# Kernel optimization log

Measured on AMD Instinct MI355X. Metric: run time of the kernel, lower is better.

Reference implementation:

```python
import jax, jax.numpy as jnp
import numpy as np

B, N, F, T, KCHEB, O = 8, 1024, 64, 12, 3, 64

def setup_inputs() -> dict:
    key = jax.random.key(0)
    k1, k2, k3, k4 = jax.random.split(key, 4)
    graph_signal = jax.random.normal(k1, (B, N, F, T), dtype=jnp.float32)
    spatial_attention = jax.random.uniform(k2, (B, N, N), dtype=jnp.float32)
    # Chebyshev polynomials of scaled Laplacian, scaled to keep magnitudes sane
    cheb = jax.random.normal(k3, (KCHEB, N, N), dtype=jnp.float32) / np.float32(np.sqrt(N))
    # theta: (K, F, num_of_filters), glorot-ish scale
    theta = jax.random.normal(k4, (KCHEB, F, O), dtype=jnp.float32) / np.float32(np.sqrt(F))
    return {"graph_signal": graph_signal, "spatial_attention": spatial_attention,
            "cheb": cheb, "theta": theta}

def reference(graph_signal, spatial_attention, cheb, theta):
    # Original loops over t and k computing:
    #   rhs[b,n,f] = sum_m (T_k[m,n] * att[b,m,n]) * x[b,m,f,t]   (transposed batch_dot)
    #   out[b,n,o,t] += rhs @ theta[k]
    # Vectorized over k, t in one pass.
    Ak = cheb[:, None, :, :] * spatial_attention[None]          # (K,B,N,N) = T_k * attention
    rhs = jnp.einsum('kbmn,bmft->kbnft', Ak, graph_signal)      # T_k_with_at^T @ x for all t
    out = jnp.einsum('kbnft,kfo->bnot', rhs, theta)             # sum over k and f
    return jax.nn.relu(out)                                     # (B, N, O, T)
```

## Files before the change

kernel.cpp:

```cpp
#include <hip/hip_runtime.h>
#include <stdint.h>

#define NB 8
#define NN 1024
#define NF 64
#define NT 12
#define NK 3
#define NO 64
#define NQ 768
#define KKC 3072

typedef __attribute__((ext_vector_type(8))) short bf16x8;
typedef __attribute__((ext_vector_type(4))) float f32x4;

typedef const unsigned int __attribute__((address_space(1)))* gas1_t;
typedef unsigned int __attribute__((address_space(3)))* las3_t;

__device__ __forceinline__ void gload_lds16(const void* g, void* l) {
  __builtin_amdgcn_global_load_lds((gas1_t)g, (las3_t)l, 16, 0, 0);
}

__device__ __forceinline__ unsigned short f2bf(float f) {
  union { float f; unsigned int u; } v; v.f = f;
  unsigned int u = v.u;
  unsigned int r = (u + 0x7FFFu + ((u >> 16) & 1u)) >> 16;
  return (unsigned short)r;
}

__global__ void k0_thetaT(const float* __restrict__ theta, unsigned short* __restrict__ thT) {
  int i = blockIdx.x * 256 + threadIdx.x;
  if (i >= NK * NO * NF) return;
  int f = i & 63, o = (i >> 6) & 63, k = i >> 12;
  thT[i] = f2bf(theta[(k * NF + f) * NO + o]);
}

__global__ __launch_bounds__(256) void k1_A2(const float* __restrict__ cheb,
                                             const float* __restrict__ att,
                                             unsigned short* __restrict__ A2) {
  __shared__ float att_s[64][65];
  __shared__ float cheb_s[64][65];
  const int n0 = blockIdx.x * 64;
  const int m0 = blockIdx.y * 64;
  const int b  = blockIdx.z;
  const int tid = threadIdx.x;
  const int r4 = tid >> 4;
  const int c  = tid & 15;

#pragma unroll
  for (int p = 0; p < 4; ++p) {
    int r = r4 + p * 16;
    const float4 v = *(const float4*)(att + ((size_t)(b * NN + m0 + r)) * NN + n0 + c * 4);
    att_s[r][c * 4 + 0] = v.x; att_s[r][c * 4 + 1] = v.y;
    att_s[r][c * 4 + 2] = v.z; att_s[r][c * 4 + 3] = v.w;
  }
  for (int k = 0; k < NK; ++k) {
#pragma unroll
    for (int p = 0; p < 4; ++p) {
      int r = r4 + p * 16;
      const float4 v = *(const float4*)(cheb + ((size_t)(k * NN + m0 + r)) * NN + n0 + c * 4);
      cheb_s[r][c * 4 + 0] = v.x; cheb_s[r][c * 4 + 1] = v.y;
      cheb_s[r][c * 4 + 2] = v.z; cheb_s[r][c * 4 + 3] = v.w;
    }
    __syncthreads();
#pragma unroll
    for (int p = 0; p < 8; ++p) {
      int e  = p * 256 + tid;
      int jn = e >> 5;
      int q  = e & 31;
      float f0 = att_s[2 * q][jn]     * cheb_s[2 * q][jn];
      float f1 = att_s[2 * q + 1][jn] * cheb_s[2 * q + 1][jn];
      unsigned int pk = (unsigned int)f2bf(f0) | ((unsigned int)f2bf(f1) << 16);
      size_t el = ((size_t)(b * NN + n0 + jn)) * KKC + k * NN + m0 + 2 * q;
      *(unsigned int*)(A2 + el) = pk;
    }
    __syncthreads();
  }
}

__global__ __launch_bounds__(256) void k2_xT(const float* __restrict__ x,
                                             unsigned short* __restrict__ xT) {
  __shared__ unsigned int lds[12][16][32];
  const int m0 = blockIdx.x * 16;
  const int b  = blockIdx.y;
  const int tid = threadIdx.x;
  const float* xb = x + ((size_t)(b * NN + m0)) * (NF * NT);

#pragma unroll
  for (int u0 = 0; u0 < 2; ++u0) {
    const int u  = u0 * 256 + tid;
    const int ml = u >> 5;
    const int fp = u & 31;
    const float* src = xb + ((size_t)ml * NF + fp * 2) * NT;
    float v[24];
#pragma unroll
    for (int i = 0; i < 6; ++i)
      *(float4*)(v + i * 4) = *(const float4*)(src + i * 4);
#pragma unroll
    for (int t = 0; t < 12; ++t) {
      unsigned int pk = (unsigned int)f2bf(v[t]) | ((unsigned int)f2bf(v[t + 12]) << 16);
      lds[t][ml][fp] = pk;
    }
  }
  __syncthreads();

#pragma unroll
  for (int it = 0; it < 12; ++it) {
    const int g = it * 256 + tid;
    const int t = g >> 8;
    const int r = g & 255;
    const int m = r >> 4;
    const int f4 = r & 15;
    uint2 u = *(const uint2*)&lds[t][m][2 * f4];
    size_t el = (((size_t)(b * NT + t) * NN) + m0 + m) * NF + f4 * 4;
    *(uint2*)(void*)(xT + el) = u;
  }
}

__global__ __launch_bounds__(256) void k3_Y(const unsigned short* __restrict__ xT,
                                            const unsigned short* __restrict__ thT,
                                            unsigned short* __restrict__ Y) {
  __shared__ unsigned short Xs[256 * 64];
  const int mc = blockIdx.x;
  const int t  = blockIdx.y;
  const int b  = blockIdx.z;
  const int tid = threadIdx.x;
  const int w = tid >> 6, l = tid & 63;
  const int lrow = l & 15, lk = l >> 4;

  const unsigned short* xbase = xT + ((size_t)(b * NT + t)) * NN * NF + (size_t)(mc * 256) * NF;

#pragma unroll
  for (int it = 0; it < 8; ++it) {
    const int idx = it * 256 + tid;
    const int r   = idx >> 3;
    const int c16 = (idx & 7) ^ (r & 7);
    gload_lds16(xbase + (size_t)r * NF + c16 * 8, Xs + (size_t)idx * 8);
  }
  __syncthreads();

  bf16x8 af[2][4];
#pragma unroll
  for (int ks = 0; ks < 2; ++ks)
#pragma unroll
    for (int mi = 0; mi < 4; ++mi) {
      const int row = w * 64 + mi * 16 + lrow;
      const int sw = (row * 128 + ks * 64 + lk * 16) ^ ((row & 7) << 4);
      af[ks][mi] = *(const bf16x8*)((const char*)Xs + sw);
    }

  for (int k = 0; k < NK; ++k) {
    const unsigned short* tb = thT + (size_t)k * NO * NF;
    f32x4 acc[4][4] = {};
#pragma unroll
    for (int ks = 0; ks < 2; ++ks) {
      bf16x8 bb[4];
#pragma unroll
      for (int oj = 0; oj < 4; ++oj)
        bb[oj] = *(const bf16x8*)(tb + (size_t)(oj * 16 + lrow) * NF + ks * 32 + lk * 8);
#pragma unroll
      for (int mi = 0; mi < 4; ++mi)
#pragma unroll
        for (int oj = 0; oj < 4; ++oj)
          acc[mi][oj] = __builtin_amdgcn_mfma_f32_16x16x32_bf16(af[ks][mi], bb[oj], acc[mi][oj], 0, 0, 0);
    }
#pragma unroll
    for (int mi = 0; mi < 4; ++mi) {
#pragma unroll
      for (int oj = 0; oj < 4; ++oj) {
        const int o  = oj * 16 + lrow;
        const int mg = mc * 256 + w * 64 + mi * 16 + lk * 4;
        uint2 u;
        u.x = (unsigned int)f2bf(acc[mi][oj][0]) | ((unsigned int)f2bf(acc[mi][oj][1]) << 16);
        u.y = (unsigned int)f2bf(acc[mi][oj][2]) | ((unsigned int)f2bf(acc[mi][oj][3]) << 16);
        size_t el = ((size_t)(b * NQ + o * NT + t)) * KKC + k * NN + mg;
        *(uint2*)(void*)(Y + el) = u;
      }
    }
  }
}

__global__ __launch_bounds__(256) void k4_main(const unsigned short* __restrict__ A2,
                                               const unsigned short* __restrict__ Y,
                                               float* __restrict__ out) {
  __shared__ unsigned short Asl[2][64 * 64];
  __shared__ unsigned short Bsl[2][128 * 64];
  const int tid = threadIdx.x;
  const int w = tid >> 6, l = tid & 63;
  const int lrow = l & 15, lk = l >> 4;
  const int wm = w >> 1, wq = w & 1;

  const int lin = (blockIdx.x & 7) * 96 + (blockIdx.x >> 3);
  const int b   = lin / 96;
  const int rem = lin % 96;
  const int bn  = rem / 6;
  const int bq  = rem % 6;

  const unsigned short* Abase = A2 + ((size_t)(b * NN + bn * 64)) * KKC;
  const unsigned short* Bbase = Y  + ((size_t)(b * NQ + bq * 128)) * KKC;

  f32x4 acc[2][4] = {};

  auto STAGE = [&](unsigned short* Ad, unsigned short* Bd, int kt) {
    const int kb = kt * 64;
#pragma unroll
    for (int it = 0; it < 2; ++it) {
      const int idx = it * 256 + tid;
      const int r   = idx >> 3;
      const int c16 = (idx & 7) ^ (r & 7);
      gload_lds16(Abase + (size_t)r * KKC + kb + c16 * 8, Ad + (size_t)idx * 8);
    }
#pragma unroll
    for (int it = 0; it < 4; ++it) {
      const int idx = it * 256 + tid;
      const int r   = idx >> 3;
      const int c16 = (idx & 7) ^ (r & 7);
      gload_lds16(Bbase + (size_t)r * KKC + kb + c16 * 8, Bd + (size_t)idx * 8);
    }
  };

  auto COMPUTE = [&](const unsigned short* As, const unsigned short* Bs) {
#pragma unroll
    for (int kss = 0; kss < 2; ++kss) {
      bf16x8 af[2], bfr[4];
#pragma unroll
      for (int mi = 0; mi < 2; ++mi) {
        const int row = wm * 32 + mi * 16 + lrow;
        const int sw = (row * 128 + kss * 64 + lk * 16) ^ ((row & 7) << 4);
        af[mi] = *(const bf16x8*)((const char*)As + sw);
      }
#pragma unroll
      for (int nj = 0; nj < 4; ++nj) {
        const int row = wq * 64 + nj * 16 + lrow;
        const int sw = (row * 128 + kss * 64 + lk * 16) ^ ((row & 7) << 4);
        bfr[nj] = *(const bf16x8*)((const char*)Bs + sw);
      }
#pragma unroll
      for (int mi = 0; mi < 2; ++mi)
#pragma unroll
        for (int nj = 0; nj < 4; ++nj)
          acc[mi][nj] = __builtin_amdgcn_mfma_f32_16x16x32_bf16(af[mi], bfr[nj], acc[mi][nj], 0, 0, 0);
    }
  };

  STAGE(Asl[0], Bsl[0], 0);
  for (int kt = 0; kt < KKC / 64; ++kt) {
    const int p = kt & 1;
    if (kt + 1 < KKC / 64) {
      STAGE(Asl[p ^ 1], Bsl[p ^ 1], kt + 1);
      asm volatile("s_waitcnt vmcnt(6)" ::: "memory");
    } else {
      asm volatile("s_waitcnt vmcnt(0)" ::: "memory");
    }
    __builtin_amdgcn_s_barrier();
    COMPUTE(Asl[p], Bsl[p]);
    __builtin_amdgcn_s_barrier();
  }

  const int nb0 = bn * 64 + wm * 32;
  const int qb0 = bq * 128 + wq * 64;
#pragma unroll
  for (int mi = 0; mi < 2; ++mi) {
#pragma unroll
    for (int nj = 0; nj < 4; ++nj) {
      const int q = qb0 + nj * 16 + lrow;
#pragma unroll
      for (int j = 0; j < 4; ++j) {
        const int n = nb0 + mi * 16 + lk * 4 + j;
        float v = acc[mi][nj][j];
        out[((size_t)(b * NN + n)) * NQ + q] = v > 0.f ? v : 0.f;
      }
    }
  }
}

extern "C" void kernel_launch(void* const* d_in, const int* in_sizes, int n_in,
                              void* d_out, int out_size, void* d_ws, size_t ws_size,
                              hipStream_t stream) {
  const float* x     = (const float*)d_in[0];
  const float* att   = (const float*)d_in[1];
  const float* cheb  = (const float*)d_in[2];
  const float* theta = (const float*)d_in[3];
  float* out = (float*)d_out;

  char* ws = (char*)d_ws;
  unsigned short* A2  = (unsigned short*)(ws);
  unsigned short* xT  = (unsigned short*)(ws + 50331648);
  unsigned short* Y   = (unsigned short*)(ws + 62914560);
  unsigned short* thT = (unsigned short*)(ws + 100663296);

  k0_thetaT<<<48, 256, 0, stream>>>(theta, thT);
  k1_A2<<<dim3(16, 16, 8), 256, 0, stream>>>(cheb, att, A2);
  k2_xT<<<dim3(64, 8), 256, 0, stream>>>(x, xT);
  k3_Y<<<dim3(4, 12, 8), 256, 0, stream>>>(xT, thT, Y);
  k4_main<<<768, 256, 0, stream>>>(A2, Y, out);
}
```

Baseline: 104.7 us.

## Reuse cheb tiles across batch in A2 build and enlarge main GEMM tiles

The A2 preparation kernel now loads all three Chebyshev tiles once per block and loops over the batch inside the block, so cheb is read from global memory once instead of once per batch. The grid shrinks from 2048 to 256 blocks. The main GEMM moves from 64x128 tiles with 256 threads to 128x192 tiles with 512 threads, giving each wave a 64x48 subtile for more operand reuse per LDS load. The trade-off is fewer blocks (256, roughly one per CU), more LDS per block, and less parallelism in the A2 kernel.

```diff
diff --git a/kernel.cpp b/kernel.cpp
--- a/kernel.cpp
+++ b/kernel.cpp
@@ -38,42 +38,46 @@
                                              const float* __restrict__ att,
                                              unsigned short* __restrict__ A2) {
   __shared__ float att_s[64][65];
-  __shared__ float cheb_s[64][65];
+  __shared__ float cheb_s[3][64][65];
   const int n0 = blockIdx.x * 64;
   const int m0 = blockIdx.y * 64;
-  const int b  = blockIdx.z;
   const int tid = threadIdx.x;
   const int r4 = tid >> 4;
   const int c  = tid & 15;
 
 #pragma unroll
-  for (int p = 0; p < 4; ++p) {
-    int r = r4 + p * 16;
-    const float4 v = *(const float4*)(att + ((size_t)(b * NN + m0 + r)) * NN + n0 + c * 4);
-    att_s[r][c * 4 + 0] = v.x; att_s[r][c * 4 + 1] = v.y;
-    att_s[r][c * 4 + 2] = v.z; att_s[r][c * 4 + 3] = v.w;
-  }
-  for (int k = 0; k < NK; ++k) {
+  for (int k = 0; k < NK; ++k)
 #pragma unroll
     for (int p = 0; p < 4; ++p) {
       int r = r4 + p * 16;
       const float4 v = *(const float4*)(cheb + ((size_t)(k * NN + m0 + r)) * NN + n0 + c * 4);
-      cheb_s[r][c * 4 + 0] = v.x; cheb_s[r][c * 4 + 1] = v.y;
-      cheb_s[r][c * 4 + 2] = v.z; cheb_s[r][c * 4 + 3] = v.w;
-    }
+      cheb_s[k][r][c * 4 + 0] = v.x; cheb_s[k][r][c * 4 + 1] = v.y;
+      cheb_s[k][r][c * 4 + 2] = v.z; cheb_s[k][r][c * 4 + 3] = v.w;
+    }
+
+  for (int b = 0; b < NB; ++b) {
     __syncthreads();
 #pragma unroll
-    for (int p = 0; p < 8; ++p) {
-      int e  = p * 256 + tid;
-      int jn = e >> 5;
-      int q  = e & 31;
-      float f0 = att_s[2 * q][jn]     * cheb_s[2 * q][jn];
-      float f1 = att_s[2 * q + 1][jn] * cheb_s[2 * q + 1][jn];
-      unsigned int pk = (unsigned int)f2bf(f0) | ((unsigned int)f2bf(f1) << 16);
-      size_t el = ((size_t)(b * NN + n0 + jn)) * KKC + k * NN + m0 + 2 * q;
-      *(unsigned int*)(A2 + el) = pk;
+    for (int p = 0; p < 4; ++p) {
+      int r = r4 + p * 16;
+      const float4 v = *(const float4*)(att + ((size_t)(b * NN + m0 + r)) * NN + n0 + c * 4);
+      att_s[r][c * 4 + 0] = v.x; att_s[r][c * 4 + 1] = v.y;
+      att_s[r][c * 4 + 2] = v.z; att_s[r][c * 4 + 3] = v.w;
     }
     __syncthreads();
+    for (int k = 0; k < NK; ++k) {
+#pragma unroll
+      for (int p = 0; p < 8; ++p) {
+        int e  = p * 256 + tid;
+        int jn = e >> 5;
+        int q  = e & 31;
+        float f0 = att_s[2 * q][jn]     * cheb_s[k][2 * q][jn];
+        float f1 = att_s[2 * q + 1][jn] * cheb_s[k][2 * q + 1][jn];
+        unsigned int pk = (unsigned int)f2bf(f0) | ((unsigned int)f2bf(f1) << 16);
+        size_t el = ((size_t)(b * NN + n0 + jn)) * KKC + k * NN + m0 + 2 * q;
+        *(unsigned int*)(A2 + el) = pk;
+      }
+    }
   }
 }
 
@@ -179,89 +183,89 @@
   }
 }
 
-__global__ __launch_bounds__(256) void k4_main(const unsigned short* __restrict__ A2,
+__global__ __launch_bounds__(512) void k4_main(const unsigned short* __restrict__ A2,
                                                const unsigned short* __restrict__ Y,
                                                float* __restrict__ out) {
-  __shared__ unsigned short Asl[2][64 * 64];
-  __shared__ unsigned short Bsl[2][128 * 64];
+  __shared__ unsigned short Asl[2][128 * 64];
+  __shared__ unsigned short Bsl[2][192 * 64];
   const int tid = threadIdx.x;
   const int w = tid >> 6, l = tid & 63;
   const int lrow = l & 15, lk = l >> 4;
-  const int wm = w >> 1, wq = w & 1;
-
-  const int lin = (blockIdx.x & 7) * 96 + (blockIdx.x >> 3);
-  const int b   = lin / 96;
-  const int rem = lin % 96;
-  const int bn  = rem / 6;
-  const int bq  = rem % 6;
-
-  const unsigned short* Abase = A2 + ((size_t)(b * NN + bn * 64)) * KKC;
-  const unsigned short* Bbase = Y  + ((size_t)(b * NQ + bq * 128)) * KKC;
-
-  f32x4 acc[2][4] = {};
-
-  auto STAGE = [&](unsigned short* Ad, unsigned short* Bd, int kt) {
+  const int wm = w >> 2, wq = w & 3;
+
+  const int lin = (blockIdx.x & 7) * 32 + (blockIdx.x >> 3);
+  const int b   = lin >> 5;
+  const int rem = lin & 31;
+  const int bn  = rem >> 2;
+  const int bq  = rem & 3;
+
+  const unsigned short* Abase = A2 + ((size_t)(b * NN + bn * 128)) * KKC;
+  const unsigned short* Bbase = Y  + ((size_t)(b * NQ + bq * 192)) * KKC;
+
+  f32x4 acc[4][3] = {};
+
+  auto STAGE = [&](int buf, int kt) {
     const int kb = kt * 64;
 #pragma unroll
     for (int it = 0; it < 2; ++it) {
-      const int idx = it * 256 + tid;
+      const int idx = it * 512 + tid;
       const int r   = idx >> 3;
       const int c16 = (idx & 7) ^ (r & 7);
-      gload_lds16(Abase + (size_t)r * KKC + kb + c16 * 8, Ad + (size_t)idx * 8);
-    }
-#pragma unroll
-    for (int it = 0; it < 4; ++it) {
-      const int idx = it * 256 + tid;
+      gload_lds16(Abase + (size_t)r * KKC + kb + c16 * 8, Asl[buf] + (size_t)idx * 8);
+    }
+#pragma unroll
+    for (int it = 0; it < 3; ++it) {
+      const int idx = it * 512 + tid;
       const int r   = idx >> 3;
       const int c16 = (idx & 7) ^ (r & 7);
-      gload_lds16(Bbase + (size_t)r * KKC + kb + c16 * 8, Bd + (size_t)idx * 8);
+      gload_lds16(Bbase + (size_t)r * KKC + kb + c16 * 8, Bsl[buf] + (size_t)idx * 8);
     }
   };
 
-  auto COMPUTE = [&](const unsigned short* As, const unsigned short* Bs) {
-#pragma unroll
-    for (int kss = 0; kss < 2; ++kss) {
-      bf16x8 af[2], bfr[4];
-#pragma unroll
-      for (int mi = 0; mi < 2; ++mi) {
-        const int row = wm * 32 + mi * 16 + lrow;
-        const int sw = (row * 128 + kss * 64 + lk * 16) ^ ((row & 7) << 4);
-        af[mi] = *(const bf16x8*)((const char*)As + sw);
-      }
-#pragma unroll
-      for (int nj = 0; nj < 4; ++nj) {
-        const int row = wq * 64 + nj * 16 + lrow;
-        const int sw = (row * 128 + kss * 64 + lk * 16) ^ ((row & 7) << 4);
-        bfr[nj] = *(const bf16x8*)((const char*)Bs + sw);
-      }
-#pragma unroll
-      for (int mi = 0; mi < 2; ++mi)
-#pragma unroll
-        for (int nj = 0; nj < 4; ++nj)
+  auto COMPUTE = [&](int buf) {
+#pragma unroll
+    for (int ks = 0; ks < 2; ++ks) {
+      bf16x8 af[4], bfr[3];
+#pragma unroll
+      for (int mi = 0; mi < 4; ++mi) {
+        const int row = wm * 64 + mi * 16 + lrow;
+        const int sw = (row * 128 + ks * 64 + lk * 16) ^ ((row & 7) << 4);
+        af[mi] = *(const bf16x8*)((const char*)Asl[buf] + sw);
+      }
+#pragma unroll
+      for (int nj = 0; nj < 3; ++nj) {
+        const int row = wq * 48 + nj * 16 + lrow;
+        const int sw = (row * 128 + ks * 64 + lk * 16) ^ ((row & 7) << 4);
+        bfr[nj] = *(const bf16x8*)((const char*)Bsl[buf] + sw);
+      }
+#pragma unroll
+      for (int mi = 0; mi < 4; ++mi)
+#pragma unroll
+        for (int nj = 0; nj < 3; ++nj)
           acc[mi][nj] = __builtin_amdgcn_mfma_f32_16x16x32_bf16(af[mi], bfr[nj], acc[mi][nj], 0, 0, 0);
     }
   };
 
-  STAGE(Asl[0], Bsl[0], 0);
+  STAGE(0, 0);
   for (int kt = 0; kt < KKC / 64; ++kt) {
     const int p = kt & 1;
     if (kt + 1 < KKC / 64) {
-      STAGE(Asl[p ^ 1], Bsl[p ^ 1], kt + 1);
-      asm volatile("s_waitcnt vmcnt(6)" ::: "memory");
+      STAGE(p ^ 1, kt + 1);
+      asm volatile("s_waitcnt vmcnt(5)" ::: "memory");
     } else {
       asm volatile("s_waitcnt vmcnt(0)" ::: "memory");
     }
     __builtin_amdgcn_s_barrier();
-    COMPUTE(Asl[p], Bsl[p]);
+    COMPUTE(p);
     __builtin_amdgcn_s_barrier();
   }
 
-  const int nb0 = bn * 64 + wm * 32;
-  const int qb0 = bq * 128 + wq * 64;
-#pragma unroll
-  for (int mi = 0; mi < 2; ++mi) {
-#pragma unroll
-    for (int nj = 0; nj < 4; ++nj) {
+  const int nb0 = bn * 128 + wm * 64;
+  const int qb0 = bq * 192 + wq * 48;
+#pragma unroll
+  for (int mi = 0; mi < 4; ++mi) {
+#pragma unroll
+    for (int nj = 0; nj < 3; ++nj) {
       const int q = qb0 + nj * 16 + lrow;
 #pragma unroll
       for (int j = 0; j < 4; ++j) {
@@ -289,8 +293,8 @@
   unsigned short* thT = (unsigned short*)(ws + 100663296);
 
   k0_thetaT<<<48, 256, 0, stream>>>(theta, thT);
-  k1_A2<<<dim3(16, 16, 8), 256, 0, stream>>>(cheb, att, A2);
+  k1_A2<<<dim3(16, 16), 256, 0, stream>>>(cheb, att, A2);
   k2_xT<<<dim3(64, 8), 256, 0, stream>>>(x, xT);
   k3_Y<<<dim3(4, 12, 8), 256, 0, stream>>>(xT, thT, Y);
-  k4_main<<<768, 256, 0, stream>>>(A2, Y, out);
-}
+  k4_main<<<256, 512, 0, stream>>>(A2, Y, out);
+}
```

Measured after the change: 113.9 us. 1.09x slower.
